# Performance work log

Measured on AMD Instinct MI355X. Metric: run time of the kernel, lower is better.

Reference implementation:

```python
import jax, jax.numpy as jnp
import numpy as np
from jax import lax

B, H, W = 8, 64, 64
C = 192          # in_channel == out_channel
CI = 384         # inner_channel = int(2.0 * C)


def setup_inputs() -> dict:
    key = jax.random.key(0)
    ks = jax.random.split(key, 8)
    s = 0.02
    return {
        "x": jax.random.normal(ks[0], (B, H, W, C), jnp.float32),
        "Win": jax.random.normal(ks[1], (C, 2 * CI), jnp.float32) * s,
        "conv_w": jax.random.normal(ks[2], (CI, 1, 3, 3), jnp.float32) * s,
        "conv_b": jnp.zeros((CI,), jnp.float32),
        "Wout": jax.random.normal(ks[3], (CI, C), jnp.float32) * s,
        "Wm1": jax.random.normal(ks[4], (C, 4 * C), jnp.float32) * s,
        "bm1": jnp.zeros((4 * C,), jnp.float32),
        "Wm2": jax.random.normal(ks[5], (4 * C, C), jnp.float32) * s,
        "bm2": jnp.zeros((C,), jnp.float32),
    }


def reference(x, Win, conv_w, conv_b, Wout, Wm1, bm1, Wm2, bm2):
    silu = jax.nn.silu
    shortcut = x                                   # [B,H,W,C], norm1 is Identity (norm=None)
    xz = jnp.einsum('bhwc,cd->bhwd', x, Win)       # in_proj (no bias) -> [B,H,W,2*CI]
    x1, z = jnp.split(xz, 2, axis=-1)
    # channel_recover -> [B,CI,H,W], depthwise conv + silu
    xc = jnp.transpose(x1, (0, 3, 1, 2))
    xc = lax.conv_general_dilated(xc, conv_w, (1, 1), 'SAME',
                                  feature_group_count=CI,
                                  dimension_numbers=('NCHW', 'OIHW', 'NCHW'))
    xc = silu(xc + conv_b[None, :, None, None])
    L = H * W
    # cross_scan: K=2 views (row-major and transposed), doubled by flip_scan -> [B,4,CI,L]
    x0 = xc.reshape(B, CI, L)
    xt = jnp.transpose(xc, (0, 1, 3, 2)).reshape(B, CI, L)
    x_cross = jnp.stack([x0, xt], axis=1)
    xs = jnp.concatenate([x_cross, jnp.flip(x_cross, axis=-1)], axis=1)
    out_y = xs  # ssm() is abstract in MBaseBlock -> identity passthrough
    # scan_proj (CrossMerge): undo flips and permutations, sum branches
    inv_y = jnp.flip(out_y[:, 2:4], axis=-1)

    def unperm(v):  # branch scanned in transposed (W,H) order -> back to (H,W)
        return jnp.transpose(v.reshape(B, CI, W, H), (0, 1, 3, 2)).reshape(B, CI, L)

    y = out_y[:, 0] + inv_y[:, 0] + unperm(out_y[:, 1]) + unperm(inv_y[:, 1])
    y = jnp.transpose(y, (0, 2, 1)).reshape(B, H, W, CI)  # norm2 is Identity
    y = y * silu(z)                                       # gate
    out = jnp.einsum('bhwc,cd->bhwd', y, Wout)            # out_proj (no bias)
    out = shortcut + out                                  # dropout/drop_path are Identity
    # dense is Identity (in_channel == out_channel); MLP branch 192->768->192
    h = silu(jnp.einsum('bhwc,cd->bhwd', out, Wm1) + bm1)
    mlp = jnp.einsum('bhwd,dc->bhwc', h, Wm2) + bm2
    return out + mlp
```

## Files before the change

### kernel.cpp

```cpp
#include <hip/hip_runtime.h>
#include <hip/hip_bf16.h>

#define BDIM 8
#define HDIM 64
#define WDIM 64
#define CDIM 192
#define CIDIM 384
#define MTOK (BDIM * HDIM * WDIM)

using bf16 = __hip_bfloat16;
typedef __attribute__((ext_vector_type(8))) short short8;
typedef __attribute__((ext_vector_type(4))) float f32x4;

__device__ __forceinline__ float silu_f(float v) { return v / (1.0f + __expf(-v)); }
__device__ __forceinline__ float bf2f(short s) {
    union { unsigned u; float f; } x; x.u = ((unsigned)(unsigned short)s) << 16; return x.f;
}

__device__ __forceinline__ void gload_lds16(const bf16* g, bf16* l) {
    __builtin_amdgcn_global_load_lds(
        (const __attribute__((address_space(1))) void*)g,
        (__attribute__((address_space(3))) void*)l, 16, 0, 0);
}

#define MFMA16(a, b, c) __builtin_amdgcn_mfma_f32_16x16x32_bf16(a, b, c, 0, 0, 0)

#define NSTRIPE 40
template <int EPI>
__launch_bounds__(256, 2)
__global__ void gemm_k192_p(const bf16* __restrict__ A, const bf16* __restrict__ BT,
                            const float* __restrict__ bias,
                            bf16* __restrict__ outB, bf16* __restrict__ outB2)
{
    __shared__ bf16 As[2][64 * 192];
    __shared__ bf16 Bs[64 * 192];

    const int bid = blockIdx.x;
    const int n   = bid / NSTRIPE;
    const int s   = bid % NSTRIPE;
    const int n0  = n * 64;

    const int tid  = threadIdx.x;
    const int lane = tid & 63;
    const int wv   = tid >> 6;
    const int wm   = wv >> 1;
    const int wn   = wv & 1;

    int soff[6];
    #pragma unroll
    for (int i = 0; i < 6; ++i) {
        const int ci   = wv * 6 + i;
        const int c    = ci * 64 + lane;
        const int row  = c / 24;
        const int slot = c - row * 24;
        const int lsl  = slot ^ (row & 7);
        soff[i] = row * 192 + lsl * 8;
    }

    #pragma unroll
    for (int i = 0; i < 6; ++i)
        gload_lds16(BT + (size_t)n0 * 192 + soff[i], &Bs[(wv * 6 + i) * 512]);
    #pragma unroll
    for (int i = 0; i < 6; ++i)
        gload_lds16(A + (size_t)(s * 64) * 192 + soff[i], &As[0][(wv * 6 + i) * 512]);
    __syncthreads();

    const int mloc[2] = { wm * 32 + (lane & 15), wm * 32 + 16 + (lane & 15) };
    const int nloc[2] = { wn * 32 + (lane & 15), wn * 32 + 16 + (lane & 15) };
    const bool isZ = (EPI == 0) && (n0 >= CIDIM);
    bf16* dst        = (EPI == 0) ? (isZ ? outB2 : outB) : outB;
    const int stride = (EPI == 0) ? CIDIM : 768;
    const int col0   = (EPI == 0) ? (isZ ? n0 - CIDIM : n0) : n0;

    int cur = 0;
    for (int mt = s; mt < 512; mt += NSTRIPE) {
        const int nmt = mt + NSTRIPE;
        if (nmt < 512) {
            const bf16* a1 = A + (size_t)(nmt * 64) * 192;
            bf16* db = As[cur ^ 1];
            #pragma unroll
            for (int i = 0; i < 6; ++i)
                gload_lds16(a1 + soff[i], &db[(wv * 6 + i) * 512]);
        }

        const bf16* la = As[cur];
        f32x4 acc[2][2] = {};
        #pragma unroll
        for (int ks = 0; ks < 6; ++ks) {
            const int t = ks * 4 + (lane >> 4);
            short8 af[2], bfr[2];
            #pragma unroll
            for (int mi = 0; mi < 2; ++mi) {
                const int m = mloc[mi];
                af[mi] = *reinterpret_cast<const short8*>(&la[m * 192 + ((t ^ (m & 7)) << 3)]);
            }
            #pragma unroll
            for (int ni = 0; ni < 2; ++ni) {
                const int nn = nloc[ni];
                bfr[ni] = *reinterpret_cast<const short8*>(&Bs[nn * 192 + ((t ^ (nn & 7)) << 3)]);
            }
            #pragma unroll
            for (int mi = 0; mi < 2; ++mi)
                #pragma unroll
                for (int ni = 0; ni < 2; ++ni)
                    acc[mi][ni] = MFMA16(af[mi], bfr[ni], acc[mi][ni]);
        }

        const int m0   = mt * 64;
        const int rowb = m0 + wm * 32 + (lane >> 4) * 4;
        const int colb = col0 + wn * 32 + (lane & 15);
        #pragma unroll
        for (int mi = 0; mi < 2; ++mi) {
            #pragma unroll
            for (int ni = 0; ni < 2; ++ni) {
                const int c = colb + ni * 16;
                #pragma unroll
                for (int j = 0; j < 4; ++j) {
                    const int row = rowb + mi * 16 + j;
                    float v = acc[mi][ni][j];
                    if constexpr (EPI == 0) {
                        if (isZ) v = 4.0f * silu_f(v);
                    } else {
                        v = silu_f(v + bias[n0 + (c - col0)]);
                    }
                    dst[(size_t)row * stride + c] = __float2bfloat16(v);
                }
            }
        }

        __syncthreads();
        cur ^= 1;
    }
}

template <int EPI>
__launch_bounds__(256, 4)
__global__ void gemm_mfma(const bf16* __restrict__ A, const bf16* __restrict__ BT,
                          const float* __restrict__ residF, bf16* __restrict__ outB,
                          int M, int N, int K, int NX)
{
    __shared__ bf16 As[128 * 64];
    __shared__ bf16 Bs[64 * 64];

    const int bid = blockIdx.x;
    const int c8  = bid & 7;
    const int kq  = bid >> 3;
    const int bx  = kq % NX;
    const int by  = (kq / NX) * 8 + c8;
    const int m0  = by * 128;
    const int n0  = bx * 64;

    const int tid  = threadIdx.x;
    const int lane = tid & 63;
    const int wv   = tid >> 6;
    const int wm   = wv >> 1;
    const int wn   = wv & 1;

    const int srow  = lane >> 3;
    const int sslot = lane & 7;

    f32x4 acc[4][2] = {};

    for (int k0 = 0; k0 < K; k0 += 64) {
        #pragma unroll
        for (int i = 0; i < 4; ++i) {
            const int rb = wv * 32 + i * 8;
            const int r  = rb + srow;
            gload_lds16(A + (size_t)(m0 + r) * K + k0 + ((sslot ^ (r & 7)) << 3),
                        &As[rb * 64]);
        }
        #pragma unroll
        for (int i = 0; i < 2; ++i) {
            const int rb = wv * 16 + i * 8;
            const int r  = rb + srow;
            gload_lds16(BT + (size_t)(n0 + r) * K + k0 + ((sslot ^ (r & 7)) << 3),
                        &Bs[rb * 64]);
        }
        __syncthreads();

        #pragma unroll
        for (int kk = 0; kk < 2; ++kk) {
            const int t = kk * 4 + (lane >> 4);
            short8 af[4], bfr[2];
            #pragma unroll
            for (int mi = 0; mi < 4; ++mi) {
                const int m = wm * 64 + mi * 16 + (lane & 15);
                af[mi] = *reinterpret_cast<const short8*>(&As[m * 64 + ((t ^ (m & 7)) << 3)]);
            }
            #pragma unroll
            for (int ni = 0; ni < 2; ++ni) {
                const int n = wn * 32 + ni * 16 + (lane & 15);
                bfr[ni] = *reinterpret_cast<const short8*>(&Bs[n * 64 + ((t ^ (n & 7)) << 3)]);
            }
            #pragma unroll
            for (int mi = 0; mi < 4; ++mi)
                #pragma unroll
                for (int ni = 0; ni < 2; ++ni)
                    acc[mi][ni] = MFMA16(af[mi], bfr[ni], acc[mi][ni]);
        }
        __syncthreads();
    }

    const int colb = n0 + wn * 32 + (lane & 15);
    const int rowb = m0 + wm * 64 + (lane >> 4) * 4;
    #pragma unroll
    for (int mi = 0; mi < 4; ++mi) {
        #pragma unroll
        for (int ni = 0; ni < 2; ++ni) {
            const int c = colb + ni * 16;
            #pragma unroll
            for (int j = 0; j < 4; ++j) {
                const int row = rowb + mi * 16 + j;
                const size_t off = (size_t)row * N + c;
                outB[off] = __float2bfloat16(acc[mi][ni][j] + residF[off]);
            }
        }
    }
}

__launch_bounds__(256, 1)
__global__ void fused_mlp(const bf16* __restrict__ ob, const bf16* __restrict__ Wm1T,
                          const bf16* __restrict__ Wm2T, const float* __restrict__ bm1,
                          const float* __restrict__ bm2, float* __restrict__ out)
{
    __shared__ bf16 obs[64 * 192];
    __shared__ bf16 hs[64 * 768];

    const int m0   = blockIdx.x * 64;
    const int tid  = threadIdx.x;
    const int lane = tid & 63;
    const int wv   = tid >> 6;
    const int l15  = lane & 15;
    const int l4   = lane >> 4;

    #pragma unroll
    for (int i = 0; i < 6; ++i) {
        const int ci   = wv * 6 + i;
        const int c    = ci * 64 + lane;
        const int row  = c / 24;
        const int slot = c - row * 24;
        gload_lds16(ob + (size_t)(m0 + row) * 192 + (slot ^ (row & 7)) * 8,
                    &obs[ci * 512]);
    }
    __syncthreads();

    #pragma unroll
    for (int cc = 0; cc < 3; ++cc) {
        const int nc = wv * 3 + cc;
        f32x4 hacc[4][4] = {};
        #pragma unroll
        for (int ks = 0; ks < 6; ++ks) {
            short8 af[4];
            #pragma unroll
            for (int mi = 0; mi < 4; ++mi) {
                const int r = mi * 16 + l15;
                af[mi] = *reinterpret_cast<const short8*>(
                    &obs[r * 192 + (((ks * 4 + l4) ^ (r & 7)) << 3)]);
            }
            #pragma unroll
            for (int ni = 0; ni < 4; ++ni) {
                const short8 b = *reinterpret_cast<const short8*>(
                    Wm1T + (size_t)(nc * 64 + ni * 16 + l15) * 192 + (ks * 4 + l4) * 8);
                #pragma unroll
                for (int mi = 0; mi < 4; ++mi)
                    hacc[mi][ni] = MFMA16(af[mi], b, hacc[mi][ni]);
            }
        }
        #pragma unroll
        for (int ni = 0; ni < 4; ++ni) {
            const int col = nc * 64 + ni * 16 + l15;
            const float bb = bm1[col];
            #pragma unroll
            for (int mi = 0; mi < 4; ++mi) {
                #pragma unroll
                for (int j = 0; j < 4; ++j) {
                    const int r  = mi * 16 + l4 * 4 + j;
                    const int ch = (col >> 3) ^ (r & 7);
                    hs[r * 768 + ch * 8 + (col & 7)] =
                        __float2bfloat16(silu_f(hacc[mi][ni][j] + bb));
                }
            }
        }
    }
    __syncthreads();

    const int c0w = wv * 48;
    f32x4 facc[4][3] = {};
    for (int ks = 0; ks < 24; ++ks) {
        short8 ha[4];
        #pragma unroll
        for (int mi = 0; mi < 4; ++mi) {
            const int r  = mi * 16 + l15;
            const int ch = (ks * 4 + l4) ^ (r & 7);
            ha[mi] = *reinterpret_cast<const short8*>(&hs[r * 768 + ch * 8]);
        }
        #pragma unroll
        for (int ni = 0; ni < 3; ++ni) {
            const short8 b = *reinterpret_cast<const short8*>(
                Wm2T + (size_t)(c0w + ni * 16 + l15) * 768 + ks * 32 + l4 * 8);
            #pragma unroll
            for (int mi = 0; mi < 4; ++mi)
                facc[mi][ni] = MFMA16(ha[mi], b, facc[mi][ni]);
        }
    }

    #pragma unroll
    for (int ni = 0; ni < 3; ++ni) {
        const int col = c0w + ni * 16 + l15;
        const float b2 = bm2[col];
        #pragma unroll
        for (int mi = 0; mi < 4; ++mi) {
            #pragma unroll
            for (int j = 0; j < 4; ++j) {
                const int r  = mi * 16 + l4 * 4 + j;
                const int ch = (col >> 3) ^ (r & 7);
                const float resid = bf2f(*reinterpret_cast<const short*>(
                    &obs[r * 192 + ch * 8 + (col & 7)]));
                out[(size_t)(m0 + r) * 192 + col] = facc[mi][ni][j] + b2 + resid;
            }
        }
    }
}

__launch_bounds__(256)
__global__ void dwconv_gate_v6(const bf16* __restrict__ x1, const bf16* __restrict__ sz,
                               const float* __restrict__ wT, const float* __restrict__ conv_b,
                               bf16* __restrict__ y)
{
    const int bid = blockIdx.x;
    const int swz = (bid & 7) * ((int)gridDim.x >> 3) + (bid >> 3);
    const int f   = swz * 256 + threadIdx.x;
    const int m   = f / 48;
    const int cg  = f - m * 48;
    const int c0  = cg * 8;
    const int h   = (m >> 6) & 63;
    const int w   = m & 63;

    float acc[8];
    {
        const f32x4 ba = *reinterpret_cast<const f32x4*>(&conv_b[c0]);
        const f32x4 bb = *reinterpret_cast<const f32x4*>(&conv_b[c0 + 4]);
        acc[0] = ba[0]; acc[1] = ba[1]; acc[2] = ba[2]; acc[3] = ba[3];
        acc[4] = bb[0]; acc[5] = bb[1]; acc[6] = bb[2]; acc[7] = bb[3];
    }

    #pragma unroll
    for (int r = 0; r < 3; ++r) {
        const int hh = h + r - 1;
        if (hh < 0 || hh >= HDIM) continue;
        #pragma unroll
        for (int dw = 0; dw < 3; ++dw) {
            const int ww = w + dw - 1;
            if (ww < 0 || ww >= WDIM) continue;
            const int mm  = m + (r - 1) * WDIM + (dw - 1);
            const int tap = r * 3 + dw;
            const short8 t = *reinterpret_cast<const short8*>(&x1[(size_t)mm * CIDIM + c0]);
            const f32x4 wa = *reinterpret_cast<const f32x4*>(&wT[tap * CIDIM + c0]);
            const f32x4 wb = *reinterpret_cast<const f32x4*>(&wT[tap * CIDIM + c0 + 4]);
            acc[0] += bf2f(t[0]) * wa[0]; acc[1] += bf2f(t[1]) * wa[1];
            acc[2] += bf2f(t[2]) * wa[2]; acc[3] += bf2f(t[3]) * wa[3];
            acc[4] += bf2f(t[4]) * wb[0]; acc[5] += bf2f(t[5]) * wb[1];
            acc[6] += bf2f(t[6]) * wb[2]; acc[7] += bf2f(t[7]) * wb[3];
        }
    }

    const short8 g = *reinterpret_cast<const short8*>(&sz[(size_t)m * CIDIM + c0]);
    bf16 tmp[8];
    #pragma unroll
    for (int j = 0; j < 8; ++j)
        tmp[j] = __float2bfloat16(silu_f(acc[j]) * bf2f(g[j]));
    *reinterpret_cast<short8*>(&y[(size_t)m * CIDIM + c0]) =
        *reinterpret_cast<const short8*>(tmp);
}

#define SZ_WIN  (192 * 768)
#define SZ_WOUT (384 * 192)
#define SZ_WM1  (192 * 768)
#define SZ_WM2  (768 * 192)
#define SZ_CW   (CIDIM * 9)
#define XCVT    (MTOK * CDIM / 4)
#define SZ_ALL  (XCVT + SZ_WIN + SZ_WOUT + SZ_WM1 + SZ_WM2 + SZ_CW)

__launch_bounds__(256)
__global__ void prep_all(const float* __restrict__ x, const float* __restrict__ Win,
                         const float* __restrict__ Wout, const float* __restrict__ Wm1,
                         const float* __restrict__ Wm2, const float* __restrict__ convw,
                         bf16* __restrict__ xb, bf16* __restrict__ WinT,
                         bf16* __restrict__ WoutT, bf16* __restrict__ Wm1T,
                         bf16* __restrict__ Wm2T, float* __restrict__ wTc)
{
    int idx = blockIdx.x * 256 + threadIdx.x;
    if (idx < XCVT) {
        const int i = idx * 4;
        const float4 v = *reinterpret_cast<const float4*>(&x[i]);
        xb[i + 0] = __float2bfloat16(v.x);
        xb[i + 1] = __float2bfloat16(v.y);
        xb[i + 2] = __float2bfloat16(v.z);
        xb[i + 3] = __float2bfloat16(v.w);
        return;
    }
    idx -= XCVT;
    if (idx < SZ_WIN) {
        const int r = idx / 768, c = idx % 768;
        WinT[(size_t)c * 192 + r] = __float2bfloat16(Win[idx]);
        return;
    }
    idx -= SZ_WIN;
    if (idx < SZ_WOUT) {
        const int r = idx / 192, c = idx % 192;
        WoutT[(size_t)c * 384 + r] = __float2bfloat16(Wout[idx]);
        return;
    }
    idx -= SZ_WOUT;
    if (idx < SZ_WM1) {
        const int r = idx / 768, c = idx % 768;
        Wm1T[(size_t)c * 192 + r] = __float2bfloat16(Wm1[idx]);
        return;
    }
    idx -= SZ_WM1;
    if (idx < SZ_WM2) {
        const int r = idx / 192, c = idx % 192;
        Wm2T[(size_t)c * 768 + r] = __float2bfloat16(Wm2[idx]);
        return;
    }
    idx -= SZ_WM2;
    if (idx < SZ_CW) {
        const int ci = idx / 9, t = idx % 9;
        wTc[t * CIDIM + ci] = convw[idx];
    }
}

extern "C" void kernel_launch(void* const* d_in, const int* in_sizes, int n_in,
                              void* d_out, int out_size, void* d_ws, size_t ws_size,
                              hipStream_t stream)
{
    const float* x      = (const float*)d_in[0];
    const float* Win    = (const float*)d_in[1];
    const float* conv_w = (const float*)d_in[2];
    const float* conv_b = (const float*)d_in[3];
    const float* Wout   = (const float*)d_in[4];
    const float* Wm1    = (const float*)d_in[5];
    const float* bm1    = (const float*)d_in[6];
    const float* Wm2    = (const float*)d_in[7];
    const float* bm2    = (const float*)d_in[8];
    float* out = (float*)d_out;

    char* ws = (char*)d_ws;
    size_t o = 0;
    bf16*  xb    = (bf16*)(ws + o); o += (size_t)MTOK * CDIM * 2;
    bf16*  WinT  = (bf16*)(ws + o); o += (size_t)768 * 192 * 2;
    bf16*  WoutT = (bf16*)(ws + o); o += (size_t)192 * 384 * 2;
    bf16*  Wm1T  = (bf16*)(ws + o); o += (size_t)768 * 192 * 2;
    bf16*  Wm2T  = (bf16*)(ws + o); o += (size_t)192 * 768 * 2;
    float* wTc   = (float*)(ws + o); o += (size_t)9 * CIDIM * 4;
    bf16*  ws_x1 = (bf16*)(ws + o); o += (size_t)MTOK * CIDIM * 2;
    bf16*  ws_sz = (bf16*)(ws + o); o += (size_t)MTOK * CIDIM * 2;
    bf16*  ws_y  = (bf16*)(ws + o); o += (size_t)MTOK * CIDIM * 2;
    bf16*  ws_ob = (bf16*)(ws + o); o += (size_t)MTOK * CDIM * 2;

    prep_all<<<dim3((SZ_ALL + 255) / 256), dim3(256), 0, stream>>>(
        x, Win, Wout, Wm1, Wm2, conv_w, xb, WinT, WoutT, Wm1T, Wm2T, wTc);

    gemm_k192_p<0><<<dim3(12 * NSTRIPE), dim3(256), 0, stream>>>(
        xb, WinT, nullptr, ws_x1, ws_sz);

    dwconv_gate_v6<<<dim3(MTOK * 48 / 256), dim3(256), 0, stream>>>(
        ws_x1, ws_sz, wTc, conv_b, ws_y);

    gemm_mfma<1><<<dim3(3 * 256), dim3(256), 0, stream>>>(
        ws_y, WoutT, x, ws_ob, MTOK, CDIM, CIDIM, 3);

    fused_mlp<<<dim3(MTOK / 64), dim3(256), 0, stream>>>(
        ws_ob, Wm1T, Wm2T, bm1, bm2, out);
}
```

Before: 137.0 us.

## Pipeline in_proj with waitcnt barriers, shrink MLP tile, fragment-order MLP weights

The in_proj GEMM now waits on vmcnt with raw s_barrier around the MMA loop and raises wave priority during compute, so the next tile's load overlaps the current one. The fused MLP kernel moves from 64-row to 32-row tiles to run more blocks per CU. Its weights are pre-packed into MFMA fragment order for coalesced loads, and the hidden buffer uses a padded stride instead of an XOR swizzle. The out_proj residual now reads the bf16 copy of x rather than fp32, which lowers memory traffic but loses some precision.

```diff
diff --git a/kernel.cpp b/kernel.cpp
--- a/kernel.cpp
+++ b/kernel.cpp
@@ -53,8 +53,7 @@
         const int c    = ci * 64 + lane;
         const int row  = c / 24;
         const int slot = c - row * 24;
-        const int lsl  = slot ^ (row & 7);
-        soff[i] = row * 192 + lsl * 8;
+        soff[i] = row * 192 + (slot ^ (row & 7)) * 8;
     }
 
     #pragma unroll
@@ -63,7 +62,6 @@
     #pragma unroll
     for (int i = 0; i < 6; ++i)
         gload_lds16(A + (size_t)(s * 64) * 192 + soff[i], &As[0][(wv * 6 + i) * 512]);
-    __syncthreads();
 
     const int mloc[2] = { wm * 32 + (lane & 15), wm * 32 + 16 + (lane & 15) };
     const int nloc[2] = { wn * 32 + (lane & 15), wn * 32 + 16 + (lane & 15) };
@@ -81,10 +79,17 @@
             #pragma unroll
             for (int i = 0; i < 6; ++i)
                 gload_lds16(a1 + soff[i], &db[(wv * 6 + i) * 512]);
-        }
+            asm volatile("s_waitcnt vmcnt(6)" ::: "memory");
+        } else {
+            asm volatile("s_waitcnt vmcnt(0)" ::: "memory");
+        }
+        __builtin_amdgcn_sched_barrier(0);
+        __builtin_amdgcn_s_barrier();
+        __builtin_amdgcn_sched_barrier(0);
 
         const bf16* la = As[cur];
         f32x4 acc[2][2] = {};
+        __builtin_amdgcn_s_setprio(1);
         #pragma unroll
         for (int ks = 0; ks < 6; ++ks) {
             const int t = ks * 4 + (lane >> 4);
@@ -105,6 +110,11 @@
                 for (int ni = 0; ni < 2; ++ni)
                     acc[mi][ni] = MFMA16(af[mi], bfr[ni], acc[mi][ni]);
         }
+        __builtin_amdgcn_s_setprio(0);
+
+        __builtin_amdgcn_sched_barrier(0);
+        __builtin_amdgcn_s_barrier();
+        __builtin_amdgcn_sched_barrier(0);
 
         const int m0   = mt * 64;
         const int rowb = m0 + wm * 32 + (lane >> 4) * 4;
@@ -127,17 +137,14 @@
                 }
             }
         }
-
-        __syncthreads();
         cur ^= 1;
     }
 }
 
-template <int EPI>
 __launch_bounds__(256, 4)
-__global__ void gemm_mfma(const bf16* __restrict__ A, const bf16* __restrict__ BT,
-                          const float* __restrict__ residF, bf16* __restrict__ outB,
-                          int M, int N, int K, int NX)
+__global__ void gemm_g3(const bf16* __restrict__ A, const bf16* __restrict__ BT,
+                        const bf16* __restrict__ residB, bf16* __restrict__ outB,
+                        int M, int N, int K, int NX)
 {
     __shared__ bf16 As[128 * 64];
     __shared__ bf16 Bs[64 * 64];
@@ -212,21 +219,23 @@
             for (int j = 0; j < 4; ++j) {
                 const int row = rowb + mi * 16 + j;
                 const size_t off = (size_t)row * N + c;
-                outB[off] = __float2bfloat16(acc[mi][ni][j] + residF[off]);
-            }
-        }
-    }
-}
-
-__launch_bounds__(256, 1)
-__global__ void fused_mlp(const bf16* __restrict__ ob, const bf16* __restrict__ Wm1T,
-                          const bf16* __restrict__ Wm2T, const float* __restrict__ bm1,
-                          const float* __restrict__ bm2, float* __restrict__ out)
-{
-    __shared__ bf16 obs[64 * 192];
-    __shared__ bf16 hs[64 * 768];
-
-    const int m0   = blockIdx.x * 64;
+                outB[off] = __float2bfloat16(acc[mi][ni][j] +
+                                             bf2f(*(const short*)&residB[off]));
+            }
+        }
+    }
+}
+
+#define HSTR 776
+__launch_bounds__(256, 2)
+__global__ void fused_mlp32(const bf16* __restrict__ ob, const bf16* __restrict__ Wm1F,
+                            const bf16* __restrict__ Wm2F, const float* __restrict__ bm1,
+                            const float* __restrict__ bm2, float* __restrict__ out)
+{
+    __shared__ bf16 obs[32 * 192];
+    __shared__ bf16 hs[32 * HSTR];
+
+    const int m0   = blockIdx.x * 32;
     const int tid  = threadIdx.x;
     const int lane = tid & 63;
     const int wv   = tid >> 6;
@@ -234,82 +243,78 @@
     const int l4   = lane >> 4;
 
     #pragma unroll
-    for (int i = 0; i < 6; ++i) {
-        const int ci   = wv * 6 + i;
+    for (int i = 0; i < 3; ++i) {
+        const int ci   = wv * 3 + i;
         const int c    = ci * 64 + lane;
         const int row  = c / 24;
         const int slot = c - row * 24;
-        gload_lds16(ob + (size_t)(m0 + row) * 192 + (slot ^ (row & 7)) * 8,
+        gload_lds16(ob + (size_t)(m0 + row) * 192 + ((slot ^ (row & 7)) << 3),
                     &obs[ci * 512]);
     }
     __syncthreads();
 
     #pragma unroll
-    for (int cc = 0; cc < 3; ++cc) {
-        const int nc = wv * 3 + cc;
-        f32x4 hacc[4][4] = {};
+    for (int g = 0; g < 3; ++g) {
+        f32x4 hacc[2][4] = {};
         #pragma unroll
         for (int ks = 0; ks < 6; ++ks) {
-            short8 af[4];
-            #pragma unroll
-            for (int mi = 0; mi < 4; ++mi) {
+            short8 af[2];
+            #pragma unroll
+            for (int mi = 0; mi < 2; ++mi) {
                 const int r = mi * 16 + l15;
                 af[mi] = *reinterpret_cast<const short8*>(
                     &obs[r * 192 + (((ks * 4 + l4) ^ (r & 7)) << 3)]);
             }
             #pragma unroll
             for (int ni = 0; ni < 4; ++ni) {
+                const int f = wv * 12 + g * 4 + ni;
                 const short8 b = *reinterpret_cast<const short8*>(
-                    Wm1T + (size_t)(nc * 64 + ni * 16 + l15) * 192 + (ks * 4 + l4) * 8);
+                    Wm1F + ((size_t)(f * 6 + ks) * 64 + lane) * 8);
                 #pragma unroll
-                for (int mi = 0; mi < 4; ++mi)
+                for (int mi = 0; mi < 2; ++mi)
                     hacc[mi][ni] = MFMA16(af[mi], b, hacc[mi][ni]);
             }
         }
         #pragma unroll
         for (int ni = 0; ni < 4; ++ni) {
-            const int col = nc * 64 + ni * 16 + l15;
+            const int col = (wv * 12 + g * 4 + ni) * 16 + l15;
             const float bb = bm1[col];
             #pragma unroll
-            for (int mi = 0; mi < 4; ++mi) {
+            for (int mi = 0; mi < 2; ++mi)
                 #pragma unroll
                 for (int j = 0; j < 4; ++j) {
-                    const int r  = mi * 16 + l4 * 4 + j;
-                    const int ch = (col >> 3) ^ (r & 7);
-                    hs[r * 768 + ch * 8 + (col & 7)] =
-                        __float2bfloat16(silu_f(hacc[mi][ni][j] + bb));
+                    const int r = mi * 16 + l4 * 4 + j;
+                    hs[r * HSTR + col] = __float2bfloat16(silu_f(hacc[mi][ni][j] + bb));
                 }
-            }
         }
     }
     __syncthreads();
 
-    const int c0w = wv * 48;
-    f32x4 facc[4][3] = {};
+    f32x4 facc[2][3] = {};
     for (int ks = 0; ks < 24; ++ks) {
-        short8 ha[4];
-        #pragma unroll
-        for (int mi = 0; mi < 4; ++mi) {
-            const int r  = mi * 16 + l15;
-            const int ch = (ks * 4 + l4) ^ (r & 7);
-            ha[mi] = *reinterpret_cast<const short8*>(&hs[r * 768 + ch * 8]);
+        short8 ha[2];
+        #pragma unroll
+        for (int mi = 0; mi < 2; ++mi) {
+            const int r = mi * 16 + l15;
+            ha[mi] = *reinterpret_cast<const short8*>(&hs[r * HSTR + ks * 32 + l4 * 8]);
         }
         #pragma unroll
         for (int ni = 0; ni < 3; ++ni) {
+            const int f = wv * 3 + ni;
             const short8 b = *reinterpret_cast<const short8*>(
-                Wm2T + (size_t)(c0w + ni * 16 + l15) * 768 + ks * 32 + l4 * 8);
-            #pragma unroll
-            for (int mi = 0; mi < 4; ++mi)
+                Wm2F + ((size_t)(f * 24 + ks) * 64 + lane) * 8);
+            #pragma unroll
+            for (int mi = 0; mi < 2; ++mi)
                 facc[mi][ni] = MFMA16(ha[mi], b, facc[mi][ni]);
         }
     }
 
     #pragma unroll
     for (int ni = 0; ni < 3; ++ni) {
-        const int col = c0w + ni * 16 + l15;
+        const int col = (wv * 3 + ni) * 16 + l15;
         const float b2 = bm2[col];
         #pragma unroll
-        for (int mi = 0; mi < 4; ++mi) {
+        for (int mi = 0; mi < 2; ++mi)
             #pragma unroll
             for (int j = 0; j < 4; ++j) {
                 const int r  = mi * 16 + l4 * 4 + j;
@@ -318,7 +323,6 @@
                     &obs[r * 192 + ch * 8 + (col & 7)]));
                 out[(size_t)(m0 + r) * 192 + col] = facc[mi][ni][j] + b2 + resid;
             }
-        }
     }
 }
 
@@ -386,8 +390,8 @@
                          const float* __restrict__ Wout, const float* __restrict__ Wm1,
                          const float* __restrict__ Wm2, const float* __restrict__ convw,
                          bf16* __restrict__ xb, bf16* __restrict__ WinT,
-                         bf16* __restrict__ WoutT, bf16* __restrict__ Wm1T,
-                         bf16* __restrict__ Wm2T, float* __restrict__ wTc)
+                         bf16* __restrict__ WoutT, bf16* __restrict__ Wm1F,
+                         bf16* __restrict__ Wm2F, float* __restrict__ wTc)
 {
     int idx = blockIdx.x * 256 + threadIdx.x;
     if (idx < XCVT) {
@@ -413,14 +417,28 @@
     }
     idx -= SZ_WOUT;
     if (idx < SZ_WM1) {
-        const int r = idx / 768, c = idx % 768;
-        Wm1T[(size_t)c * 192 + r] = __float2bfloat16(Wm1[idx]);
+        const int f  = idx / 3072;
+        const int r1 = idx - f * 3072;
+        const int ks = r1 / 512;
+        const int r2 = r1 - ks * 512;
+        const int l  = r2 >> 3;
+        const int e  = r2 & 7;
+        const int row = f * 16 + (l & 15);
+        const int k   = ks * 32 + (l >> 4) * 8 + e;
+        Wm1F[idx] = __float2bfloat16(Wm1[(size_t)k * 768 + row]);
         return;
     }
     idx -= SZ_WM1;
     if (idx < SZ_WM2) {
-        const int r = idx / 192, c = idx % 192;
-        Wm2T[(size_t)c * 768 + r] = __float2bfloat16(Wm2[idx]);
+        const int f  = idx / 12288;
+        const int r1 = idx - f * 12288;
+        const int ks = r1 / 512;
+        const int r2 = r1 - ks * 512;
+        const int l  = r2 >> 3;
+        const int e  = r2 & 7;
+        const int row = f * 16 + (l & 15);
+        const int k   = ks * 32 + (l >> 4) * 8 + e;
+        Wm2F[idx] = __float2bfloat16(Wm2[(size_t)k * 192 + row]);
         return;
     }
     idx -= SZ_WM2;
@@ -450,8 +468,8 @@
     bf16*  xb    = (bf16*)(ws + o); o += (size_t)MTOK * CDIM * 2;
     bf16*  WinT  = (bf16*)(ws + o); o += (size_t)768 * 192 * 2;
     bf16*  WoutT = (bf16*)(ws + o); o += (size_t)192 * 384 * 2;
-    bf16*  Wm1T  = (bf16*)(ws + o); o += (size_t)768 * 192 * 2;
-    bf16*  Wm2T  = (bf16*)(ws + o); o += (size_t)192 * 768 * 2;
+    bf16*  Wm1F  = (bf16*)(ws + o); o += (size_t)SZ_WM1 * 2;
+    bf16*  Wm2F  = (bf16*)(ws + o); o += (size_t)SZ_WM2 * 2;
     float* wTc   = (float*)(ws + o); o += (size_t)9 * CIDIM * 4;
     bf16*  ws_x1 = (bf16*)(ws + o); o += (size_t)MTOK * CIDIM * 2;
     bf16*  ws_sz = (bf16*)(ws + o); o += (size_t)MTOK * CIDIM * 2;
@@ -459,7 +477,7 @@
     bf16*  ws_ob = (bf16*)(ws + o); o += (size_t)MTOK * CDIM * 2;
 
     prep_all<<<dim3((SZ_ALL + 255) / 256), dim3(256), 0, stream>>>(
-        x, Win, Wout, Wm1, Wm2, conv_w, xb, WinT, WoutT, Wm1T, Wm2T, wTc);
+        x, Win, Wout, Wm1, Wm2, conv_w, xb, WinT, WoutT, Wm1F, Wm2F, wTc);
 
     gemm_k192_p<0><<<dim3(12 * NSTRIPE), dim3(256), 0, stream>>>(
         xb, WinT, nullptr, ws_x1, ws_sz);
@@ -467,9 +485,9 @@
     dwconv_gate_v6<<<dim3(MTOK * 48 / 256), dim3(256), 0, stream>>>(
         ws_x1, ws_sz, wTc, conv_b, ws_y);
 
-    gemm_mfma<1><<<dim3(3 * 256), dim3(256), 0, stream>>>(
-        ws_y, WoutT, x, ws_ob, MTOK, CDIM, CIDIM, 3);
-
-    fused_mlp<<<dim3(MTOK / 64), dim3(256), 0, stream>>>(
-        ws_ob, Wm1T, Wm2T, bm1, bm2, out);
-}
+    gemm_g3<<<dim3(3 * 256), dim3(256), 0, stream>>>(
+        ws_y, WoutT, xb, ws_ob, MTOK, CDIM, CIDIM, 3);
+
+    fused_mlp32<<<dim3(MTOK / 32), dim3(256), 0, stream>>>(
+        ws_ob, Wm1F, Wm2F, bm1, bm2, out);
+}
```

Result: faster. 117.1 us, median of 3 (-14.5%).
